# Optimization experiments

Measured on AMD Instinct MI355X. Metric: run time of the kernel, lower is better.

The kernel has to match this reference:

```python
import jax, jax.numpy as jnp
import numpy as np

DIM = 1024
HEADS = 16
HEAD_DIM = DIM // HEADS
EPS = 1e-5


def _layer_norm(z, g, b):
    m = jnp.mean(z, axis=-1, keepdims=True)
    v = jnp.var(z, axis=-1, keepdims=True)
    return (z - m) * jax.lax.rsqrt(v + EPS) * g + b


def setup_inputs() -> dict:
    key = jax.random.key(0)
    ks = jax.random.split(key, 8)
    B, T, S = 2, 2048, 2048
    x = jax.random.normal(ks[0], (B, T, DIM), dtype=jnp.float32)
    context = jax.random.normal(ks[1], (B, S, DIM), dtype=jnp.float32)
    w_qkv = jax.random.normal(ks[2], (DIM, 3 * DIM), dtype=jnp.float32) * 0.02
    b_qkv = jnp.zeros((3 * DIM,), dtype=jnp.float32)
    w_out = jax.random.normal(ks[3], (DIM, DIM), dtype=jnp.float32) * 0.02
    b_out = jnp.zeros((DIM,), dtype=jnp.float32)
    ln_g = jnp.ones((DIM,), dtype=jnp.float32)
    ln_b = jnp.zeros((DIM,), dtype=jnp.float32)
    return {"x": x, "context": context, "w_qkv": w_qkv, "b_qkv": b_qkv,
            "w_out": w_out, "b_out": b_out, "ln_g": ln_g, "ln_b": ln_b}


def reference(x, context, w_qkv, b_qkv, w_out, b_out, ln_g, ln_b):
    B, T, C = x.shape
    S = context.shape[1]
    scale = HEAD_DIM ** -0.5

    def split_heads(z):  # [B, L, C] -> [B, H, L, Dh]
        return z.reshape(z.shape[0], z.shape[1], HEADS, HEAD_DIM).transpose(0, 2, 1, 3)

    # self qkv
    qkv = _layer_norm(x, ln_g, ln_b) @ w_qkv + b_qkv  # [B, T, 3C]
    q = split_heads(qkv[..., :C])
    k = split_heads(qkv[..., C:2 * C])
    v = split_heads(qkv[..., 2 * C:])

    # context k, v from the shared qkv projection (K/V slices)
    ckv = _layer_norm(context, ln_g, ln_b) @ w_qkv + b_qkv  # [B, S, 3C]
    ck = split_heads(ckv[..., C:2 * C])
    cv = split_heads(ckv[..., 2 * C:])

    k = jnp.concatenate([k, ck], axis=2)  # [B, H, T+S, Dh]
    v = jnp.concatenate([v, cv], axis=2)

    attn = jax.nn.softmax(jnp.einsum('bhtd,bhsd->bhts', q, k) * scale, axis=-1)
    out = jnp.einsum('bhts,bhsd->bhtd', attn, v)  # [B, H, T, Dh]
    out = out.transpose(0, 2, 1, 3).reshape(B, T, C)
    return out @ w_out + b_out + x
```

## Files before the change

kernel.cpp:

```cpp
#include <hip/hip_runtime.h>
#include <stdint.h>

#define H 16
#define DH 64
#define T 2048
#define SS 2048
#define L 4096
#define DIM 1024
#define BB 2

typedef __bf16 bf16x8 __attribute__((ext_vector_type(8)));
typedef float f32x4 __attribute__((ext_vector_type(4)));
typedef float f32x16 __attribute__((ext_vector_type(16)));
typedef unsigned u32x4 __attribute__((ext_vector_type(4)));

__device__ __forceinline__ unsigned short f2bf(float f){
  unsigned u = __builtin_bit_cast(unsigned, f);
  u += 0x7fff + ((u >> 16) & 1);
  return (unsigned short)(u >> 16);
}

__device__ __forceinline__ unsigned cvt_pk_bf16(float lo, float hi){
  unsigned r;
  asm("v_cvt_pk_bf16_f32 %0, %1, %2" : "=v"(r) : "v"(lo), "v"(hi));
  return r;
}

__device__ __forceinline__ float fmax3(float a, float b, float c){
  float r;
  asm("v_max3_f32 %0, %1, %2, %3" : "=v"(r) : "v"(a), "v"(b), "v"(c));
  return r;
}

__device__ __forceinline__ void gload_lds16(const void* g, void* l){
  void* gnc = const_cast<void*>(g);
  __builtin_amdgcn_global_load_lds((__attribute__((address_space(1))) void*)gnc,
                                   (__attribute__((address_space(3))) void*)l, 16, 0, 0);
}

__global__ __launch_bounds__(256) void ln_kernel(const float* __restrict__ x, const float* __restrict__ ctx,
                          const float* __restrict__ g, const float* __restrict__ b,
                          unsigned short* __restrict__ out){
  int row = blockIdx.x;
  int tid = threadIdx.x;
  const float* src = (row < BB*T) ? (x + (size_t)row*DIM) : (ctx + (size_t)(row - BB*T)*DIM);
  float4 v = reinterpret_cast<const float4*>(src)[tid];
  float s  = v.x + v.y + v.z + v.w;
  float s2 = v.x*v.x + v.y*v.y + v.z*v.z + v.w*v.w;
  #pragma unroll
  for (int off = 32; off > 0; off >>= 1){
    s  += __shfl_down(s,  off, 64);
    s2 += __shfl_down(s2, off, 64);
  }
  __shared__ float red[8];
  if ((tid & 63) == 0){ red[(tid>>6)*2] = s; red[(tid>>6)*2+1] = s2; }
  __syncthreads();
  s  = red[0] + red[2] + red[4] + red[6];
  s2 = red[1] + red[3] + red[5] + red[7];
  float mean = s * (1.0f/DIM);
  float var  = s2 * (1.0f/DIM) - mean*mean;
  float rstd = rsqrtf(var + 1e-5f);
  float4 gg = reinterpret_cast<const float4*>(g)[tid];
  float4 bv = reinterpret_cast<const float4*>(b)[tid];
  ushort4 o;
  o.x = f2bf((v.x-mean)*rstd*gg.x + bv.x);
  o.y = f2bf((v.y-mean)*rstd*gg.y + bv.y);
  o.z = f2bf((v.z-mean)*rstd*gg.z + bv.z);
  o.w = f2bf((v.w-mean)*rstd*gg.w + bv.w);
  reinterpret_cast<ushort4*>(out + (size_t)row*DIM)[tid] = o;
}

__global__ __launch_bounds__(256) void transpose_f32_bf16(const float* __restrict__ in,
                          unsigned short* __restrict__ out, int R, int C){
  __shared__ float tile[32][33];
  int c0 = blockIdx.x*32, r0 = blockIdx.y*32;
  int tx = threadIdx.x, ty = threadIdx.y;
  #pragma unroll
  for (int k = 0; k < 4; k++)
    tile[ty + k*8][tx] = in[(size_t)(r0 + ty + k*8)*C + c0 + tx];
  __syncthreads();
  #pragma unroll
  for (int k = 0; k < 4; k++)
    out[(size_t)(c0 + ty + k*8)*R + r0 + tx] = f2bf(tile[tx][ty + k*8]);
}

__global__ __launch_bounds__(256) void qkv_gemm(const unsigned short* __restrict__ A,
      const unsigned short* __restrict__ Bt, const float* __restrict__ bias,
      unsigned short* __restrict__ qbuf, unsigned short* __restrict__ kbuf,
      unsigned short* __restrict__ vtbuf){
  int orig = blockIdx.x;
  int wid = (orig & 7)*192 + (orig >> 3);
  int n0 = (wid % 24)*128, m0 = (wid / 24)*128;
  if (m0 >= BB*T && n0 < DIM) return;
  __shared__ unsigned short at[128*32];
  __shared__ unsigned short btile[128*32];
  int tid = threadIdx.x, lane = tid & 63, wv = tid >> 6;
  int wm = (wv >> 1)*64, wn = (wv & 1)*64;
  f32x4 acc[4][4];
  #pragma unroll
  for (int i = 0; i < 4; i++)
    #pragma unroll
    for (int j = 0; j < 4; j++) acc[i][j] = (f32x4){0.f,0.f,0.f,0.f};

  for (int k0 = 0; k0 < DIM; k0 += 32){
    #pragma unroll
    for (int c = 0; c < 2; c++){
      int idx = c*256 + tid;
      int row = idx >> 2, koff = (idx & 3)*16;
      gload_lds16((const char*)A  + ((size_t)(m0+row)*DIM + k0)*2 + koff,
                  (char*)at + (c*256 + wv*64)*16);
      gload_lds16((const char*)Bt + ((size_t)(n0+row)*DIM + k0)*2 + koff,
                  (char*)btile + (c*256 + wv*64)*16);
    }
    __syncthreads();
    bf16x8 af[4], bfv[4];
    #pragma unroll
    for (int i = 0; i < 4; i++){
      af[i]  = *reinterpret_cast<const bf16x8*>((const char*)at    + (wm + i*16 + (lane&15))*64 + (lane>>4)*16);
      bfv[i] = *reinterpret_cast<const bf16x8*>((const char*)btile + (wn + i*16 + (lane&15))*64 + (lane>>4)*16);
    }
    #pragma unroll
    for (int mi = 0; mi < 4; mi++)
      #pragma unroll
      for (int ni = 0; ni < 4; ni++)
        acc[mi][ni] = __builtin_amdgcn_mfma_f32_16x16x32_bf16(af[mi], bfv[ni], acc[mi][ni], 0,0,0);
    __syncthreads();
  }

  #pragma unroll
  for (int ni = 0; ni < 4; ni++){
    int gn = n0 + wn + ni*16 + (lane & 15);
    float bv = bias[gn];
    int sec = gn >> 10, cc = gn & 1023, hh = cc >> 6, d = cc & 63;
    #pragma unroll
    for (int mi = 0; mi < 4; mi++){
      int gmb = m0 + wm + mi*16 + ((lane >> 4) << 2);
      bool isctx = gmb >= BB*T;
      int rm = isctx ? gmb - BB*T : gmb;
      int bidx = rm >> 11, tt = rm & 2047;
      size_t bh = (size_t)bidx*H + hh;
      if (sec == 0){
        if (isctx) continue;
        #pragma unroll
        for (int r = 0; r < 4; r++)
          qbuf[(bh*T + tt + r)*DH + d] = f2bf((acc[mi][ni][r] + bv)*0.18033688f);
      } else if (sec == 1){
        int j = isctx ? T + tt : tt;
        #pragma unroll
        for (int r = 0; r < 4; r++)
          kbuf[(bh*L + j + r)*DH + d] = f2bf(acc[mi][ni][r] + bv);
      } else {
        int j = isctx ? T + tt : tt;
        ushort4 o;
        o.x = f2bf(acc[mi][ni][0] + bv);
        o.y = f2bf(acc[mi][ni][1] + bv);
        o.z = f2bf(acc[mi][ni][2] + bv);
        o.w = f2bf(acc[mi][ni][3] + bv);
        *reinterpret_cast<ushort4*>(vtbuf + (bh*DH + d)*L + j) = o;
      }
    }
  }
}

__global__ __launch_bounds__(256) void attn_kernel(const unsigned short* __restrict__ q,
      const unsigned short* __restrict__ kbuf, const unsigned short* __restrict__ vtbuf,
      unsigned short* __restrict__ ao){
  int hw = blockIdx.x;
  int wid = (hw & 7)*64 + (hw >> 3);
  int qt = wid & 15, hb = wid >> 4;
  int hh = hb & 15, b = hb >> 4;
  int tid = threadIdx.x, lane = tid & 63, wv = tid >> 6;
  int hi = lane >> 5, q32 = lane & 31;
  __shared__ unsigned short kt[2][128*64];
  __shared__ unsigned short vtt[2][64*128];
  size_t bh = (size_t)b*H + hh;
  int qbase = qt*128 + wv*32;

  const unsigned short* qp = q + (bh*T + qbase + q32)*DH + hi*8;
  bf16x8 qf[4];
  #pragma unroll
  for (int ks = 0; ks < 4; ks++)
    qf[ks] = *reinterpret_cast<const bf16x8*>(qp + ks*16);

  bf16x8 ones;
  #pragma unroll
  for (int j = 0; j < 8; j++) ones[j] = (__bf16)1.0f;

  f32x16 o_acc[2], l_vec;
  #pragma unroll
  for (int d = 0; d < 2; d++)
    #pragma unroll
    for (int i = 0; i < 16; i++) o_acc[d][i] = 0.f;
  #pragma unroll
  for (int i = 0; i < 16; i++) l_vec[i] = 0.f;
  float m_l = -1e30f;

  const char* kg = (const char*)(kbuf + bh*(size_t)L*DH);
  const char* vg = (const char*)(vtbuf + bh*(size_t)DH*L);

  #define STAGE(bufi, jt) { \
    _Pragma("unroll") \
    for (int c = 0; c < 4; c++){ \
      int idx = c*256 + tid; \
      int krow = idx >> 3, kc = idx & 7; \
      gload_lds16(kg + (size_t)((jt)*128 + krow)*128 + ((kc ^ (krow & 7))*16), \
                  (char*)kt[bufi] + (c*256 + wv*64)*16); \
      int vrow = idx >> 4, vc = idx & 15; \
      gload_lds16(vg + (size_t)vrow*(L*2) + (jt)*256 + ((vc ^ (vrow & 7))*16), \
                  (char*)vtt[bufi] + (c*256 + wv*64)*16); \
    } }

  STAGE(0, 0);
  __syncthreads();

  for (int jt = 0; jt < L/128; ++jt){
    int bufi = jt & 1;
    if (jt + 1 < L/128) STAGE(bufi^1, jt+1);
    const char* kb = (const char*)kt[bufi];
    const char* vb = (const char*)vtt[bufi];

    f32x16 sc[4];
    #pragma unroll
    for (int t = 0; t < 4; t++)
      #pragma unroll
      for (int i = 0; i < 16; i++) sc[t][i] = 0.f;
    #pragma unroll
    for (int ks = 0; ks < 4; ks++){
      #pragma unroll
      for (int t = 0; t < 4; t++){
        int row = t*32 + q32;
        bf16x8 kf = *reinterpret_cast<const bf16x8*>(kb + row*128 + (((ks*2+hi) ^ (row&7))*16));
        sc[t] = __builtin_amdgcn_mfma_f32_32x32x16_bf16(kf, qf[ks], sc[t], 0,0,0);
      }
    }

    float rt[4];
    #pragma unroll
    for (int t = 0; t < 4; t++){
      float v0 = fmax3(sc[t][0],  sc[t][1],  sc[t][2]);
      float v1 = fmax3(sc[t][3],  sc[t][4],  sc[t][5]);
      float v2 = fmax3(sc[t][6],  sc[t][7],  sc[t][8]);
      float v3 = fmax3(sc[t][9],  sc[t][10], sc[t][11]);
      float v4 = fmax3(sc[t][12], sc[t][13], sc[t][14]);
      rt[t] = fmaxf(fmax3(v0, v1, v2), fmax3(v3, v4, sc[t][15]));
    }
    float tm = fmaxf(fmax3(rt[0], rt[1], rt[2]), rt[3]);

    if (!__all(tm - m_l <= 8.0f)){
      float tmf = fmaxf(tm, __shfl_xor(tm, 32, 64));
      float mn = fmaxf(m_l, tmf);
      float alpha = exp2f(m_l - mn);
      m_l = mn;
      #pragma unroll
      for (int d = 0; d < 2; d++)
        #pragma unroll
        for (int i = 0; i < 16; i++) o_acc[d][i] *= alpha;
      l_vec[0] *= alpha;
    }
    #pragma unroll
    for (int t = 0; t < 4; t++)
      #pragma unroll
      for (int i = 0; i < 16; i++)
        sc[t][i] = exp2f(sc[t][i] - m_l);

    bf16x8 pfrag[8];
    #pragma unroll
    for (int t = 0; t < 4; t++){
      #pragma unroll
      for (int half = 0; half < 2; half++){
        unsigned p01 = cvt_pk_bf16(sc[t][half*8+0], sc[t][half*8+1]);
        unsigned p23 = cvt_pk_bf16(sc[t][half*8+2], sc[t][half*8+3]);
        unsigned p45 = cvt_pk_bf16(sc[t][half*8+4], sc[t][half*8+5]);
        unsigned p67 = cvt_pk_bf16(sc[t][half*8+6], sc[t][half*8+7]);
        asm("v_permlane32_swap_b32 %0, %1" : "+v"(p01), "+v"(p45));
        asm("v_permlane32_swap_b32 %0, %1" : "+v"(p23), "+v"(p67));
        u32x4 w = (u32x4){p01, p23, p45, p67};
        pfrag[t*2 + half] = __builtin_bit_cast(bf16x8, w);
      }
    }

    #pragma unroll
    for (int ks = 0; ks < 8; ks++){
      #pragma unroll
      for (int d = 0; d < 2; d++){
        int row = d*32 + q32;
        bf16x8 vf = *reinterpret_cast<const bf16x8*>(vb + row*256 + (((ks*2+hi) ^ (row&7))*16));
        o_acc[d] = __builtin_amdgcn_mfma_f32_32x32x16_bf16(vf, pfrag[ks], o_acc[d], 0,0,0);
      }
      l_vec = __builtin_amdgcn_mfma_f32_32x32x16_bf16(ones, pfrag[ks], l_vec, 0,0,0);
    }
    __syncthreads();
  }

  float inv = 1.0f / l_vec[0];
  unsigned short* aop = ao + ((size_t)b*T + qbase + q32)*DIM + hh*DH;
  #pragma unroll
  for (int d = 0; d < 2; d++)
    #pragma unroll
    for (int rg = 0; rg < 4; rg++){
      int d0 = d*32 + rg*8 + hi*4;
      ushort4 o;
      o.x = __builtin_bit_cast(unsigned short, (__bf16)(o_acc[d][rg*4+0]*inv));
      o.y = __builtin_bit_cast(unsigned short, (__bf16)(o_acc[d][rg*4+1]*inv));
      o.z = __builtin_bit_cast(unsigned short, (__bf16)(o_acc[d][rg*4+2]*inv));
      o.w = __builtin_bit_cast(unsigned short, (__bf16)(o_acc[d][rg*4+3]*inv));
      *reinterpret_cast<ushort4*>(aop + d0) = o;
    }
}

__global__ __launch_bounds__(256) void out_gemm(const unsigned short* __restrict__ A,
      const unsigned short* __restrict__ Bt, const float* __restrict__ bout,
      const float* __restrict__ xres, float* __restrict__ out){
  int n0 = blockIdx.x*128, m0 = blockIdx.y*128;
  __shared__ unsigned short at[128*32];
  __shared__ unsigned short btile[128*32];
  int tid = threadIdx.x, lane = tid & 63, wv = tid >> 6;
  int wm = (wv >> 1)*64, wn = (wv & 1)*64;
  f32x4 acc[4][4];
  #pragma unroll
  for (int i = 0; i < 4; i++)
    #pragma unroll
    for (int j = 0; j < 4; j++) acc[i][j] = (f32x4){0.f,0.f,0.f,0.f};

  for (int k0 = 0; k0 < DIM; k0 += 32){
    #pragma unroll
    for (int c = 0; c < 2; c++){
      int idx = c*256 + tid;
      int row = idx >> 2, koff = (idx & 3)*16;
      gload_lds16((const char*)A  + ((size_t)(m0+row)*DIM + k0)*2 + koff,
                  (char*)at + (c*256 + wv*64)*16);
      gload_lds16((const char*)Bt + ((size_t)(n0+row)*DIM + k0)*2 + koff,
                  (char*)btile + (c*256 + wv*64)*16);
    }
    __syncthreads();
    bf16x8 af[4], bfv[4];
    #pragma unroll
    for (int i = 0; i < 4; i++){
      af[i]  = *reinterpret_cast<const bf16x8*>((const char*)at    + (wm + i*16 + (lane&15))*64 + (lane>>4)*16);
      bfv[i] = *reinterpret_cast<const bf16x8*>((const char*)btile + (wn + i*16 + (lane&15))*64 + (lane>>4)*16);
    }
    #pragma unroll
    for (int mi = 0; mi < 4; mi++)
      #pragma unroll
      for (int ni = 0; ni < 4; ni++)
        acc[mi][ni] = __builtin_amdgcn_mfma_f32_16x16x32_bf16(af[mi], bfv[ni], acc[mi][ni], 0,0,0);
    __syncthreads();
  }

  #pragma unroll
  for (int ni = 0; ni < 4; ni++){
    int gn = n0 + wn + ni*16 + (lane & 15);
    float bv = bout[gn];
    #pragma unroll
    for (int mi = 0; mi < 4; mi++){
      int gmb = m0 + wm + mi*16 + ((lane >> 4) << 2);
      #pragma unroll
      for (int r = 0; r < 4; r++){
        int gm = gmb + r;
        out[(size_t)gm*DIM + gn] = acc[mi][ni][r] + bv + xres[(size_t)gm*DIM + gn];
      }
    }
  }
}

extern "C" void kernel_launch(void* const* d_in, const int* in_sizes, int n_in,
                              void* d_out, int out_size, void* d_ws, size_t ws_size,
                              hipStream_t stream){
  const float* x    = (const float*)d_in[0];
  const float* ctx  = (const float*)d_in[1];
  const float* wqkv = (const float*)d_in[2];
  const float* bqkv = (const float*)d_in[3];
  const float* wout = (const float*)d_in[4];
  const float* bout = (const float*)d_in[5];
  const float* lng  = (const float*)d_in[6];
  const float* lnb  = (const float*)d_in[7];
  float* out = (float*)d_out;

  char* ws = (char*)d_ws;
  unsigned short* wqkvT  = (unsigned short*)ws; ws += (size_t)3072*1024*2;
  unsigned short* woutT  = (unsigned short*)ws; ws += (size_t)1024*1024*2;
  unsigned short* ln_all = (unsigned short*)ws; ws += (size_t)8192*1024*2;
  unsigned short* qbuf   = (unsigned short*)ws; ws += (size_t)BB*H*T*DH*2;
  unsigned short* kbuf   = (unsigned short*)ws; ws += (size_t)BB*H*L*DH*2;
  unsigned short* vtbuf  = (unsigned short*)ws; ws += (size_t)BB*H*DH*L*2;
  unsigned short* aobuf  = (unsigned short*)ws; ws += (size_t)BB*T*DIM*2;

  transpose_f32_bf16<<<dim3(3072/32, 1024/32), dim3(32,8), 0, stream>>>(wqkv, wqkvT, 1024, 3072);
  transpose_f32_bf16<<<dim3(1024/32, 1024/32), dim3(32,8), 0, stream>>>(wout, woutT, 1024, 1024);
  ln_kernel<<<dim3(8192), dim3(256), 0, stream>>>(x, ctx, lng, lnb, ln_all);
  qkv_gemm<<<dim3(1536), dim3(256), 0, stream>>>(ln_all, wqkvT, bqkv, qbuf, kbuf, vtbuf);
  attn_kernel<<<dim3(512), dim3(256), 0, stream>>>(qbuf, kbuf, vtbuf, aobuf);
  out_gemm<<<dim3(1024/128, 4096/128), dim3(256), 0, stream>>>(aobuf, woutT, bout, x, out);
}
```

Measured before the change: 250.6 us.

## Split attention KV range across two blocks and combine partials

Splits the key/value length into two halves, one block per half, doubling the grid to 1024 blocks. Each block writes its normalized partial output plus running max and sum, and a new combine kernel merges the two halves with log-sum-exp weights. The KV tile shrinks from 128 to 64 rows to halve LDS, launch bounds ask for 4 blocks per CU, and exp2f is replaced with the hardware exp2 intrinsic. This trades more parallelism and occupancy for an extra kernel launch, an extra round trip of partial results through memory, and partials rounded to bf16 before the merge. Workspace buffers that are no longer needed at that point are reused to hold the partials.

```diff
diff --git a/kernel.cpp b/kernel.cpp
--- a/kernel.cpp
+++ b/kernel.cpp
@@ -162,21 +162,21 @@
   }
 }
 
-__global__ __launch_bounds__(256) void attn_kernel(const unsigned short* __restrict__ q,
+__global__ __launch_bounds__(256, 4) void attn_kernel(const unsigned short* __restrict__ q,
       const unsigned short* __restrict__ kbuf, const unsigned short* __restrict__ vtbuf,
-      unsigned short* __restrict__ ao){
+      unsigned short* __restrict__ obuf, float* __restrict__ mbuf, float* __restrict__ lbuf){
   int hw = blockIdx.x;
-  int wid = (hw & 7)*64 + (hw >> 3);
-  int qt = wid & 15, hb = wid >> 4;
-  int hh = hb & 15, b = hb >> 4;
+  int wid = (hw & 7)*128 + (hw >> 3);
+  int qt = wid & 15, bh = (wid >> 4) & 31, cb = wid >> 9;
+  int hh = bh & 15, b = bh >> 4;
   int tid = threadIdx.x, lane = tid & 63, wv = tid >> 6;
   int hi = lane >> 5, q32 = lane & 31;
-  __shared__ unsigned short kt[2][128*64];
-  __shared__ unsigned short vtt[2][64*128];
-  size_t bh = (size_t)b*H + hh;
+  __shared__ unsigned short kt[2][64*64];
+  __shared__ unsigned short vtt[2][64*64];
+  size_t bhs = (size_t)b*H + hh;
   int qbase = qt*128 + wv*32;
 
-  const unsigned short* qp = q + (bh*T + qbase + q32)*DH + hi*8;
+  const unsigned short* qp = q + (bhs*T + qbase + q32)*DH + hi*8;
   bf16x8 qf[4];
   #pragma unroll
   for (int ks = 0; ks < 4; ks++)
@@ -195,48 +195,48 @@
   for (int i = 0; i < 16; i++) l_vec[i] = 0.f;
   float m_l = -1e30f;
 
-  const char* kg = (const char*)(kbuf + bh*(size_t)L*DH);
-  const char* vg = (const char*)(vtbuf + bh*(size_t)DH*L);
+  const char* kg = (const char*)(kbuf + bhs*(size_t)L*DH) + (size_t)cb*2048*128;
+  const char* vg = (const char*)(vtbuf + bhs*(size_t)DH*L) + (size_t)cb*4096;
 
   #define STAGE(bufi, jt) { \
     _Pragma("unroll") \
-    for (int c = 0; c < 4; c++){ \
+    for (int c = 0; c < 2; c++){ \
       int idx = c*256 + tid; \
-      int krow = idx >> 3, kc = idx & 7; \
-      gload_lds16(kg + (size_t)((jt)*128 + krow)*128 + ((kc ^ (krow & 7))*16), \
+      int row = idx >> 3, c16 = idx & 7; \
+      int sc16 = c16 ^ (row & 7); \
+      gload_lds16(kg + (size_t)((jt)*64 + row)*128 + sc16*16, \
                   (char*)kt[bufi] + (c*256 + wv*64)*16); \
-      int vrow = idx >> 4, vc = idx & 15; \
-      gload_lds16(vg + (size_t)vrow*(L*2) + (jt)*256 + ((vc ^ (vrow & 7))*16), \
+      gload_lds16(vg + (size_t)row*(L*2) + (jt)*128 + sc16*16, \
                   (char*)vtt[bufi] + (c*256 + wv*64)*16); \
     } }
 
   STAGE(0, 0);
   __syncthreads();
 
-  for (int jt = 0; jt < L/128; ++jt){
+  for (int jt = 0; jt < 32; ++jt){
     int bufi = jt & 1;
-    if (jt + 1 < L/128) STAGE(bufi^1, jt+1);
+    if (jt + 1 < 32) STAGE(bufi^1, jt+1);
     const char* kb = (const char*)kt[bufi];
     const char* vb = (const char*)vtt[bufi];
 
-    f32x16 sc[4];
-    #pragma unroll
-    for (int t = 0; t < 4; t++)
+    f32x16 sc[2];
+    #pragma unroll
+    for (int t = 0; t < 2; t++)
       #pragma unroll
       for (int i = 0; i < 16; i++) sc[t][i] = 0.f;
     #pragma unroll
     for (int ks = 0; ks < 4; ks++){
       #pragma unroll
-      for (int t = 0; t < 4; t++){
+      for (int t = 0; t < 2; t++){
         int row = t*32 + q32;
         bf16x8 kf = *reinterpret_cast<const bf16x8*>(kb + row*128 + (((ks*2+hi) ^ (row&7))*16));
         sc[t] = __builtin_amdgcn_mfma_f32_32x32x16_bf16(kf, qf[ks], sc[t], 0,0,0);
       }
     }
 
-    float rt[4];
-    #pragma unroll
-    for (int t = 0; t < 4; t++){
+    float rt[2];
+    #pragma unroll
+    for (int t = 0; t < 2; t++){
       float v0 = fmax3(sc[t][0],  sc[t][1],  sc[t][2]);
       float v1 = fmax3(sc[t][3],  sc[t][4],  sc[t][5]);
       float v2 = fmax3(sc[t][6],  sc[t][7],  sc[t][8]);
@@ -244,12 +244,12 @@
       float v4 = fmax3(sc[t][12], sc[t][13], sc[t][14]);
       rt[t] = fmaxf(fmax3(v0, v1, v2), fmax3(v3, v4, sc[t][15]));
     }
-    float tm = fmaxf(fmax3(rt[0], rt[1], rt[2]), rt[3]);
+    float tm = fmaxf(rt[0], rt[1]);
 
     if (!__all(tm - m_l <= 8.0f)){
       float tmf = fmaxf(tm, __shfl_xor(tm, 32, 64));
       float mn = fmaxf(m_l, tmf);
-      float alpha = exp2f(m_l - mn);
+      float alpha = __builtin_amdgcn_exp2f(m_l - mn);
       m_l = mn;
       #pragma unroll
       for (int d = 0; d < 2; d++)
@@ -258,14 +258,14 @@
       l_vec[0] *= alpha;
     }
     #pragma unroll
-    for (int t = 0; t < 4; t++)
+    for (int t = 0; t < 2; t++)
       #pragma unroll
       for (int i = 0; i < 16; i++)
-        sc[t][i] = exp2f(sc[t][i] - m_l);
-
-    bf16x8 pfrag[8];
-    #pragma unroll
-    for (int t = 0; t < 4; t++){
+        sc[t][i] = __builtin_amdgcn_exp2f(sc[t][i] - m_l);
+
+    bf16x8 pfrag[4];
+    #pragma unroll
+    for (int t = 0; t < 2; t++){
       #pragma unroll
       for (int half = 0; half < 2; half++){
         unsigned p01 = cvt_pk_bf16(sc[t][half*8+0], sc[t][half*8+1]);
@@ -280,11 +280,11 @@
     }
 
     #pragma unroll
-    for (int ks = 0; ks < 8; ks++){
+    for (int ks = 0; ks < 4; ks++){
       #pragma unroll
       for (int d = 0; d < 2; d++){
         int row = d*32 + q32;
-        bf16x8 vf = *reinterpret_cast<const bf16x8*>(vb + row*256 + (((ks*2+hi) ^ (row&7))*16));
+        bf16x8 vf = *reinterpret_cast<const bf16x8*>(vb + row*128 + (((ks*2+hi) ^ (row&7))*16));
         o_acc[d] = __builtin_amdgcn_mfma_f32_32x32x16_bf16(vf, pfrag[ks], o_acc[d], 0,0,0);
       }
       l_vec = __builtin_amdgcn_mfma_f32_32x32x16_bf16(ones, pfrag[ks], l_vec, 0,0,0);
@@ -293,7 +293,7 @@
   }
 
   float inv = 1.0f / l_vec[0];
-  unsigned short* aop = ao + ((size_t)b*T + qbase + q32)*DIM + hh*DH;
+  unsigned short* aop = obuf + (size_t)cb*BB*H*T*DH + ((size_t)bh*T + qbase + q32)*DH;
   #pragma unroll
   for (int d = 0; d < 2; d++)
     #pragma unroll
@@ -306,6 +306,38 @@
       o.w = __builtin_bit_cast(unsigned short, (__bf16)(o_acc[d][rg*4+3]*inv));
       *reinterpret_cast<ushort4*>(aop + d0) = o;
     }
+  if (hi == 0){
+    size_t mi = ((size_t)cb*BB*H + bh)*T + qbase + q32;
+    mbuf[mi] = m_l;
+    lbuf[mi] = l_vec[0];
+  }
+}
+
+__global__ __launch_bounds__(256) void attn_combine(const unsigned short* __restrict__ obuf,
+      const float* __restrict__ mbuf, const float* __restrict__ lbuf,
+      unsigned short* __restrict__ ao){
+  int gid = blockIdx.x*256 + threadIdx.x;
+  int d8 = gid & 7;
+  int qg = gid >> 3;
+  int qq = qg & (T-1);
+  int bh = qg >> 11;
+  int b = bh >> 4, h = bh & 15;
+  float m0 = mbuf[(size_t)qg];
+  float m1 = mbuf[(size_t)BB*H*T + qg];
+  float l0 = lbuf[(size_t)qg];
+  float l1 = lbuf[(size_t)BB*H*T + qg];
+  float mm = fmaxf(m0, m1);
+  float w0 = l0 * __builtin_amdgcn_exp2f(m0 - mm);
+  float w1 = l1 * __builtin_amdgcn_exp2f(m1 - mm);
+  float inv = 1.0f / (w0 + w1);
+  w0 *= inv; w1 *= inv;
+  bf16x8 o0 = *reinterpret_cast<const bf16x8*>(obuf + (size_t)qg*DH + d8*8);
+  bf16x8 o1 = *reinterpret_cast<const bf16x8*>(obuf + (size_t)BB*H*T*DH + (size_t)qg*DH + d8*8);
+  bf16x8 res;
+  #pragma unroll
+  for (int j = 0; j < 8; j++)
+    res[j] = (__bf16)(w0*(float)o0[j] + w1*(float)o1[j]);
+  *reinterpret_cast<bf16x8*>(ao + ((size_t)b*T + qq)*DIM + h*DH + d8*8) = res;
 }
 
 __global__ __launch_bounds__(256) void out_gemm(const unsigned short* __restrict__ A,
@@ -385,10 +417,15 @@
   unsigned short* vtbuf  = (unsigned short*)ws; ws += (size_t)BB*H*DH*L*2;
   unsigned short* aobuf  = (unsigned short*)ws; ws += (size_t)BB*T*DIM*2;
 
+  unsigned short* obuf = ln_all;
+  float* mbuf = (float*)wqkvT;
+  float* lbuf = mbuf + (size_t)2*BB*H*T;
+
   transpose_f32_bf16<<<dim3(3072/32, 1024/32), dim3(32,8), 0, stream>>>(wqkv, wqkvT, 1024, 3072);
   transpose_f32_bf16<<<dim3(1024/32, 1024/32), dim3(32,8), 0, stream>>>(wout, woutT, 1024, 1024);
   ln_kernel<<<dim3(8192), dim3(256), 0, stream>>>(x, ctx, lng, lnb, ln_all);
   qkv_gemm<<<dim3(1536), dim3(256), 0, stream>>>(ln_all, wqkvT, bqkv, qbuf, kbuf, vtbuf);
-  attn_kernel<<<dim3(512), dim3(256), 0, stream>>>(qbuf, kbuf, vtbuf, aobuf);
+  attn_kernel<<<dim3(1024), dim3(256), 0, stream>>>(qbuf, kbuf, vtbuf, obuf, mbuf, lbuf);
+  attn_combine<<<dim3(BB*H*T*8/256), dim3(256), 0, stream>>>(obuf, mbuf, lbuf, aobuf);
   out_gemm<<<dim3(1024/128, 4096/128), dim3(256), 0, stream>>>(aobuf, woutT, bout, x, out);
 }
```

Result: faster. 222.4 us (-11.3%).
